# Performance work log

Hardware: AMD Instinct MI355X
Metric: run time of the kernel (lower is better)

Reference implementation:

```python
import jax, jax.numpy as jnp
import numpy as np

EMBED_DIM = 2048
NUM_HEADS = 16
HEAD_DIM = EMBED_DIM // NUM_HEADS  # 128
D_K = 128
SCALE = 1.0 / float(np.sqrt(HEAD_DIM))
LAYER_DEPTH = 6 / 12  # amrpa_layer_idx / n_amrpa_layers
BATCH, SEQ = 2, 2048


def setup_inputs() -> dict:
    key = jax.random.key(0)
    ks = jax.random.split(key, 8)
    return {
        "hidden_states": jax.random.normal(ks[0], (BATCH, SEQ, EMBED_DIM), jnp.float32),
        "c_attn_w": jax.random.normal(ks[1], (EMBED_DIM, 3 * EMBED_DIM), jnp.float32) * 0.02,
        "c_attn_b": jax.random.normal(ks[2], (3 * EMBED_DIM,), jnp.float32) * 0.02,
        "c_proj_w": jax.random.normal(ks[3], (EMBED_DIM, EMBED_DIM), jnp.float32) * 0.02,
        "c_proj_b": jax.random.normal(ks[4], (EMBED_DIM,), jnp.float32) * 0.02,
        "cam_gate": jax.random.normal(ks[5], (D_K,), jnp.float32) * 0.1,
        "cam_w0": jax.random.normal(ks[6], (1,), jnp.float32),
        "cam_w1": jax.random.normal(ks[7], (1,), jnp.float32),
    }


def reference(hidden_states, c_attn_w, c_attn_b, c_proj_w, c_proj_b, cam_gate, cam_w0, cam_w1):
    # GPT2 Conv1D-style fused QKV projection: [B,S,3E]
    qkv = hidden_states @ c_attn_w + c_attn_b
    Q, K, V = jnp.split(qkv, 3, axis=2)  # each [B,S,E]
    # NOTE: faithful to source — attention over the FULL embed dim (no head split),
    # scaled by 1/sqrt(head_dim); causal mask is computed but never applied upstream.
    attn_scores = jnp.einsum('bse,bte->bst', Q, K) * SCALE  # [B,S,S]

    # CAM: sliced low-rank channels
    Q_cam, K_cam, V_cam = Q[:, :, :D_K], K[:, :, :D_K], V[:, :, :D_K]
    # base attention map computed under no_grad in the original
    base_A = jax.lax.stop_gradient(
        jax.nn.softmax(jnp.einsum('bsd,btd->bst', Q_cam, K_cam) * SCALE, axis=-1))
    layer_weight = jax.nn.sigmoid(cam_w0[0] + cam_w1[0] * LAYER_DEPTH)
    cam_ctx = jnp.einsum('bst,btd->bsd', base_A, V_cam)            # [B,S,d_k]
    cam_bias = jnp.einsum('bsd,btd->bst', jnp.tanh(cam_ctx * cam_gate), K_cam)
    cam_bias = cam_bias * (SCALE * layer_weight)                   # cam_mask is all-ones

    final_attn = jax.nn.softmax(attn_scores + cam_bias, axis=-1)
    context = jnp.einsum('bst,bte->bse', final_attn, V)            # [B,S,E]
    output = context @ c_proj_w + c_proj_b                         # resid_dropout is identity (eval)
    return output
```

## Files before the change

kernel.cpp:

```cpp
#include <hip/hip_runtime.h>
#include <hip/hip_bf16.h>

typedef unsigned short u16;
typedef __attribute__((ext_vector_type(8))) __bf16 bf16x8;
typedef __attribute__((ext_vector_type(4))) float f32x4;
typedef __attribute__((ext_vector_type(4))) unsigned short u16x4;

#define SCALE_QK 0.08838834764831845f

__device__ __forceinline__ u16 f2bf(float x) {
  union { float f; unsigned u; } v; v.f = x;
  unsigned r = v.u + 0x7fffu + ((v.u >> 16) & 1u);
  return (u16)(r >> 16);
}

__device__ __forceinline__ void gload_lds16(const u16* g, u16* l) {
  __builtin_amdgcn_global_load_lds(
      (const __attribute__((address_space(1))) unsigned*)g,
      (__attribute__((address_space(3))) unsigned*)l, 16, 0, 0);
}

#define CFENCE() asm volatile("" ::: "memory")
#define WAITV(N) asm volatile("s_waitcnt vmcnt(" #N ")" ::: "memory")

template<bool OUT_BF16, bool HAS_BIAS, bool TWO_SEG>
__global__ __launch_bounds__(512, 2)
void g128q(const u16* __restrict__ A1, int lda1, long sA1,
           const u16* __restrict__ B1, int ldb1, long sB1, int K1,
           const u16* __restrict__ A2, int lda2, long sA2,
           const u16* __restrict__ B2, int ldb2, long sB2, int K2,
           void* __restrict__ Cv, int ldc, long sC,
           float scale, const float* __restrict__ bias, int nbx,
           int mapmode, u16* __restrict__ vTout)
{
  extern __shared__ u16 lds[];
  const int bz = blockIdx.z;
  const int nwg = gridDim.x, orig = blockIdx.x;
  const int q8 = nwg >> 3, r8 = nwg & 7;
  const int xcd = orig & 7, lp = orig >> 3;
  const int wg = (xcd < r8 ? xcd * (q8 + 1) : r8 * (q8 + 1) + (xcd - r8) * q8) + lp;
  int bx, by;
  if (mapmode == 1) {
    const int x = wg / 96, c = wg % 96;
    const int rect = c / 48, i6 = c % 48;
    by = rect * 8 + (i6 & 7);
    bx = x * 6 + (i6 >> 3);
  } else {
    by = wg / nbx; bx = wg % nbx;
  }
  const long m0 = (long)by * 256, n0 = (long)bx * 128;

  const int tid = threadIdx.x, wid = tid >> 6, lane = tid & 63;
  const int wm = wid >> 1, wn = wid & 1;
  const int rl = lane & 15, g = lane >> 4;
  const int xa = rl & 7;
  const int uk0 = ((g ^ xa) << 3);
  const int uk1 = (((4 + g) ^ xa) << 3);

  int aoffb[4], boffb[4];
#pragma unroll
  for (int i = 0; i < 4; ++i) aoffb[i] = (wm * 64 + i * 16 + rl) * 64;
#pragma unroll
  for (int j = 0; j < 4; ++j) boffb[j] = 16384 + (wn * 64 + j * 16 + rl) * 64;

  const int ra = tid >> 3;
  const int xcol = (((tid & 7) ^ ((tid >> 3) & 7)) << 3);

  f32x4 acc[4][4];
#pragma unroll
  for (int i = 0; i < 4; ++i)
#pragma unroll
    for (int j = 0; j < 4; ++j) acc[i][j] = (f32x4){0.f, 0.f, 0.f, 0.f};

  bf16x8 av[2][4], bv[2][2];

#define STG(T_, BO_) { const int k0_ = (T_) << 6;                        \
    gload_lds16(Ab + (long)(ra      ) * lda + k0_ + xcol, lds + (BO_) +         tid * 8); \
    gload_lds16(Ab + (long)(ra +  64) * lda + k0_ + xcol, lds + (BO_) +  4096 + tid * 8); \
    gload_lds16(Ab + (long)(ra + 128) * lda + k0_ + xcol, lds + (BO_) +  8192 + tid * 8); \
    gload_lds16(Ab + (long)(ra + 192) * lda + k0_ + xcol, lds + (BO_) + 12288 + tid * 8); \
    gload_lds16(Bb + (long)(ra      ) * ldb + k0_ + xcol, lds + (BO_) + 16384 + tid * 8); \
    gload_lds16(Bb + (long)(ra +  64) * ldb + k0_ + xcol, lds + (BO_) + 20480 + tid * 8); }
#define RD0(BO_) { const u16* p_ = lds + (BO_);                          \
    _Pragma("unroll") for (int i_ = 0; i_ < 4; ++i_) {                   \
      av[0][i_] = *(const bf16x8*)(p_ + aoffb[i_] + uk0);                \
      av[1][i_] = *(const bf16x8*)(p_ + aoffb[i_] + uk1); }              \
    _Pragma("unroll") for (int j_ = 0; j_ < 2; ++j_) {                   \
      bv[0][j_] = *(const bf16x8*)(p_ + boffb[j_] + uk0);                \
      bv[1][j_] = *(const bf16x8*)(p_ + boffb[j_] + uk1); } }
#define RD1(BO_) { const u16* p_ = lds + (BO_);                          \
    _Pragma("unroll") for (int j_ = 0; j_ < 2; ++j_) {                   \
      bv[0][j_] = *(const bf16x8*)(p_ + boffb[2 + j_] + uk0);            \
      bv[1][j_] = *(const bf16x8*)(p_ + boffb[2 + j_] + uk1); } }
#define MMPH(JB_)                                                        \
    CFENCE(); __builtin_amdgcn_s_barrier();                              \
    asm volatile("s_waitcnt lgkmcnt(0)" ::: "memory");                   \
    __builtin_amdgcn_sched_barrier(0);                                   \
    __builtin_amdgcn_s_setprio(1);                                       \
    _Pragma("unroll") for (int k_ = 0; k_ < 2; ++k_)                     \
      _Pragma("unroll") for (int i_ = 0; i_ < 4; ++i_)                   \
        _Pragma("unroll") for (int j_ = 0; j_ < 2; ++j_)                 \
          acc[i_][(JB_) + j_] = __builtin_amdgcn_mfma_f32_16x16x32_bf16( \
              av[k_][i_], bv[k_][j_], acc[i_][(JB_) + j_], 0, 0, 0);     \
    __builtin_amdgcn_s_setprio(0);                                       \
    CFENCE(); __builtin_amdgcn_s_barrier(); CFENCE();

  const int NSEG = TWO_SEG ? 2 : 1;
#pragma unroll 1
  for (int seg = 0; seg < NSEG; ++seg) {
    const int lda = (seg == 0) ? lda1 : lda2;
    const int ldb = (seg == 0) ? ldb1 : ldb2;
    const int K   = (seg == 0) ? K1 : K2;
    const u16* Ab = ((seg == 0) ? A1 + (long)bz * sA1 : A2 + (long)bz * sA2) + m0 * (long)lda;
    const u16* Bb = ((seg == 0) ? B1 + (long)bz * sB1 : B2 + (long)bz * sB2) + n0 * (long)ldb;
    const int NT = K >> 6;

    STG(0, 0); STG(1, 24576);
    WAITV(6);
    CFENCE(); __builtin_amdgcn_s_barrier(); CFENCE();

    int bo = 0;
#pragma unroll 1
    for (int t = 0; t < NT; ++t) {
      RD0(bo);
      if (t + 2 < NT) {
        int bos = bo - 24576; if (bos < 0) bos = 49152;
        STG(t + 2, bos);
        WAITV(6);
      } else if (t + 1 < NT) {
        WAITV(0);
      }
      MMPH(0)
      RD1(bo);
      MMPH(2)
      bo += 24576; if (bo == 73728) bo = 0;
    }
  }
#undef STG
#undef RD0
#undef RD1
#undef MMPH

  const int r0 = (lane >> 4) << 2;
  const int cL = lane & 15;
#pragma unroll
  for (int i = 0; i < 4; ++i) {
#pragma unroll
    for (int j = 0; j < 4; ++j) {
      const long row = m0 + wm * 64 + i * 16 + r0;
      const long col = n0 + wn * 64 + j * 16 + cL;
      float bvs = 0.f;
      if (HAS_BIAS) bvs = bias[col];
      if (OUT_BF16) {
        u16* Cp = (u16*)Cv + (long)bz * sC;
        if (vTout && col >= 4096) {
          u16x4 tq;
#pragma unroll
          for (int r = 0; r < 4; ++r) tq[r] = f2bf(acc[i][j][r] * scale + bvs);
          *(u16x4*)(vTout + ((long)(row >> 11) * 2048 + (col - 4096)) * 2048 + (row & 2047)) = tq;
        } else {
#pragma unroll
          for (int r = 0; r < 4; ++r)
            Cp[(row + r) * ldc + col] = f2bf(acc[i][j][r] * scale + bvs);
        }
      } else {
        float* Cp = (float*)Cv + (long)bz * sC;
#pragma unroll
        for (int r = 0; r < 4; ++r)
          Cp[(row + r) * ldc + col] = acc[i][j][r] * scale + bvs;
      }
    }
  }
}

__global__ __launch_bounds__(256)
void gemm_bt_splitk(const u16* __restrict__ A, int lda, long sA,
                    const u16* __restrict__ B, int ldb, long sB,
                    float* __restrict__ C, int ldc, long sC,
                    int Kslice, float scale)
{
  __shared__ u16 As[128 * 64];
  __shared__ u16 Bs[128 * 64];
  const int ks = blockIdx.z & 7;
  const int bz = blockIdx.z >> 3;
  const u16* Ap  = A + (long)bz * sA + ks * Kslice;
  const u16* Bp  = B + (long)bz * sB + ks * Kslice;
  const int tid  = threadIdx.x;
  const int wid  = tid >> 6;
  const int lane = tid & 63;
  const long m0  = (long)blockIdx.y * 128;
  const long n0  = (long)blockIdx.x * 128;
  const int lrow = lane >> 3;
  const int lk   = (lane & 7) << 3;
  const int wr   = wid >> 1, wc = wid & 1;

  f32x4 acc[4][4];
#pragma unroll
  for (int i = 0; i < 4; ++i)
#pragma unroll
    for (int j = 0; j < 4; ++j) acc[i][j] = (f32x4){0.f, 0.f, 0.f, 0.f};

  for (int k0 = 0; k0 < Kslice; k0 += 64) {
#pragma unroll
    for (int c4 = 0; c4 < 4; ++c4) {
      const int chunk = (wid << 2) + c4;
      gload_lds16(Ap + (m0 + (chunk << 3) + lrow) * lda + k0 + lk, &As[chunk << 9]);
      gload_lds16(Bp + (n0 + (chunk << 3) + lrow) * ldb + k0 + lk, &Bs[chunk << 9]);
    }
    __syncthreads();
#pragma unroll
    for (int kk = 0; kk < 2; ++kk) {
      bf16x8 af[4], bfr[4];
      const int kof   = (kk << 5) + ((lane >> 4) << 3);
      const int rbase = lane & 15;
#pragma unroll
      for (int i = 0; i < 4; ++i)
        af[i] = *(const bf16x8*)&As[(((wr << 6) + (i << 4) + rbase) << 6) + kof];
#pragma unroll
      for (int j = 0; j < 4; ++j)
        bfr[j] = *(const bf16x8*)&Bs[(((wc << 6) + (j << 4) + rbase) << 6) + kof];
#pragma unroll
      for (int i = 0; i < 4; ++i)
#pragma unroll
        for (int j = 0; j < 4; ++j)
          acc[i][j] = __builtin_amdgcn_mfma_f32_16x16x32_bf16(af[i], bfr[j], acc[i][j], 0, 0, 0);
    }
    __syncthreads();
  }

  const int r0 = (lane >> 4) << 2;
  const int cL = lane & 15;
  float* Cp = C + (long)bz * sC;
#pragma unroll
  for (int i = 0; i < 4; ++i) {
#pragma unroll
    for (int j = 0; j < 4; ++j) {
      const long row = m0 + (wr << 6) + (i << 4) + r0;
      const long col = n0 + (wc << 6) + (j << 4) + cL;
#pragma unroll
      for (int r = 0; r < 4; ++r)
        atomicAdd(&Cp[(row + r) * ldc + col], acc[i][j][r] * scale);
    }
  }
}

__global__ __launch_bounds__(256)
void softmax_rows2048(const float* __restrict__ src, u16* __restrict__ dst) {
  const long row = blockIdx.x;
  const float4* s = (const float4*)(src + row * 2048);
  const int tid = threadIdx.x;
  float4 a = s[tid * 2], b = s[tid * 2 + 1];
  float m = fmaxf(fmaxf(fmaxf(a.x, a.y), fmaxf(a.z, a.w)),
                  fmaxf(fmaxf(b.x, b.y), fmaxf(b.z, b.w)));
#pragma unroll
  for (int o = 32; o > 0; o >>= 1) m = fmaxf(m, __shfl_xor(m, o));
  __shared__ float redm[4];
  __shared__ float reds[4];
  if ((tid & 63) == 0) redm[tid >> 6] = m;
  __syncthreads();
  m = fmaxf(fmaxf(redm[0], redm[1]), fmaxf(redm[2], redm[3]));
  float e[8];
  e[0] = __expf(a.x - m); e[1] = __expf(a.y - m); e[2] = __expf(a.z - m); e[3] = __expf(a.w - m);
  e[4] = __expf(b.x - m); e[5] = __expf(b.y - m); e[6] = __expf(b.z - m); e[7] = __expf(b.w - m);
  float sum = e[0] + e[1] + e[2] + e[3] + e[4] + e[5] + e[6] + e[7];
#pragma unroll
  for (int o = 32; o > 0; o >>= 1) sum += __shfl_xor(sum, o);
  if ((tid & 63) == 0) reds[tid >> 6] = sum;
  __syncthreads();
  sum = reds[0] + reds[1] + reds[2] + reds[3];
  const float inv = 1.f / sum;
  u16x4 o1 = { f2bf(e[0] * inv), f2bf(e[1] * inv), f2bf(e[2] * inv), f2bf(e[3] * inv) };
  u16x4 o2 = { f2bf(e[4] * inv), f2bf(e[5] * inv), f2bf(e[6] * inv), f2bf(e[7] * inv) };
  u16x4* d = (u16x4*)(dst + row * 2048);
  d[tid * 2]     = o1;
  d[tid * 2 + 1] = o2;
}

__global__ void transpose_f32_to_bf16(const float* __restrict__ src, u16* __restrict__ dst,
                                      int R, int C) {
  __shared__ float t[32][33];
  const int c0 = blockIdx.x * 32, r0 = blockIdx.y * 32;
  const int tx = threadIdx.x, ty = threadIdx.y;
#pragma unroll
  for (int i = 0; i < 4; ++i)
    t[ty + i * 8][tx] = src[(long)(r0 + ty + i * 8) * C + c0 + tx];
  __syncthreads();
#pragma unroll
  for (int i = 0; i < 4; ++i)
    dst[(long)(c0 + ty + i * 8) * R + r0 + tx] = f2bf(t[tx][ty + i * 8]);
}

__global__ __launch_bounds__(256)
void convert_f32_to_bf16(const float* __restrict__ src, u16* __restrict__ dst, long n4) {
  long i = (long)blockIdx.x * 256 + threadIdx.x;
  if (i < n4) {
    float4 v = ((const float4*)src)[i];
    *(u16x4*)(dst + i * 4) = (u16x4){ f2bf(v.x), f2bf(v.y), f2bf(v.z), f2bf(v.w) };
  }
}

__global__ __launch_bounds__(256)
void cam_tanh_kernel(const float* __restrict__ ctx, const float* __restrict__ gate,
                     const float* __restrict__ w0, const float* __restrict__ w1,
                     u16* __restrict__ out, int n) {
  int i = blockIdx.x * 256 + threadIdx.x;
  if (i < n) {
    const float lw = 1.f / (1.f + __expf(-(w0[0] + 0.5f * w1[0])));
    int d = i & 127;
    out[i] = f2bf(tanhf(ctx[i] * gate[d]) * lw);
  }
}

__global__ __launch_bounds__(256)
void zero_f32(float* __restrict__ p, int n) {
  int i = blockIdx.x * 256 + threadIdx.x;
  if (i < n) p[i] = 0.f;
}

extern "C" void kernel_launch(void* const* d_in, const int* in_sizes, int n_in,
                              void* d_out, int out_size, void* d_ws, size_t ws_size,
                              hipStream_t stream) {
  const float* hs       = (const float*)d_in[0];
  const float* c_attn_w = (const float*)d_in[1];
  const float* c_attn_b = (const float*)d_in[2];
  const float* c_proj_w = (const float*)d_in[3];
  const float* c_proj_b = (const float*)d_in[4];
  const float* cam_gate = (const float*)d_in[5];
  const float* cam_w0   = (const float*)d_in[6];
  const float* cam_w1   = (const float*)d_in[7];
  float* out = (float*)d_out;

  char* w = (char*)d_ws;
  u16*   hs_b    = (u16*)(w + 256);
  u16*   waT_b   = (u16*)(w + 256 + 16777216UL);
  u16*   wpT_b   = (u16*)(w + 256 + 41943040UL);
  u16*   qkv_b   = (u16*)(w + 256 + 50331648UL);
  u16*   vT_b    = (u16*)(w + 256 + 100663296UL);
  float* scoresF = (float*)(w + 256 + 117440512UL);
  float* camS    = (float*)(w + 256 + 150994944UL);
  float* ctxF    = (float*)(w + 256 + 184549376UL);
  u16*   camT_b  = (u16*)(w + 256 + 186646528UL);
  u16* baseA_b = hs_b;
  u16* P_b     = (u16*)camS;
  u16* ctxE_b  = (u16*)scoresF;

  dim3 b256(256);
  const int LDSB = 147456;

  hipFuncSetAttribute((const void*)g128q<true, true, false>,
                      hipFuncAttributeMaxDynamicSharedMemorySize, LDSB);
  hipFuncSetAttribute((const void*)g128q<false, false, false>,
                      hipFuncAttributeMaxDynamicSharedMemorySize, LDSB);
  hipFuncSetAttribute((const void*)g128q<false, false, true>,
                      hipFuncAttributeMaxDynamicSharedMemorySize, LDSB);
  hipFuncSetAttribute((const void*)g128q<true, false, false>,
                      hipFuncAttributeMaxDynamicSharedMemorySize, LDSB);
  hipFuncSetAttribute((const void*)g128q<false, true, false>,
                      hipFuncAttributeMaxDynamicSharedMemorySize, LDSB);

  convert_f32_to_bf16<<<dim3(8192), b256, 0, stream>>>(hs, hs_b, 2097152L);
  transpose_f32_to_bf16<<<dim3(192, 64), dim3(32, 8), 0, stream>>>(c_attn_w, waT_b, 2048, 6144);
  transpose_f32_to_bf16<<<dim3(64, 64), dim3(32, 8), 0, stream>>>(c_proj_w, wpT_b, 2048, 2048);

  g128q<true, true, false><<<dim3(768, 1, 1), dim3(512), LDSB, stream>>>(
      hs_b, 2048, 0L, waT_b, 2048, 0L, 2048,
      nullptr, 0, 0L, nullptr, 0, 0L, 0,
      qkv_b, 6144, 0L, 1.f, c_attn_b, 48, 1, vT_b);

  g128q<false, false, false><<<dim3(128, 1, 2), dim3(512), LDSB, stream>>>(
      qkv_b, 6144, 2048L * 6144, qkv_b + 2048, 6144, 2048L * 6144, 128,
      nullptr, 0, 0L, nullptr, 0, 0L, 0,
      camS, 2048, 2048L * 2048, SCALE_QK, nullptr, 16, 0, nullptr);

  softmax_rows2048<<<dim3(4096), b256, 0, stream>>>(camS, baseA_b);

  zero_f32<<<dim3(2048), b256, 0, stream>>>(ctxF, 524288);
  gemm_bt_splitk<<<dim3(1, 16, 16), b256, 0, stream>>>(
      baseA_b, 2048, 2048L * 2048, vT_b, 2048, 2048L * 2048,
      ctxF, 128, 2048L * 128, 256, 1.f);

  cam_tanh_kernel<<<dim3(2048), b256, 0, stream>>>(ctxF, cam_gate, cam_w0, cam_w1,
                                                   camT_b, 524288);

  g128q<false, false, true><<<dim3(128, 1, 2), dim3(512), LDSB, stream>>>(
      qkv_b, 6144, 2048L * 6144, qkv_b + 2048, 6144, 2048L * 6144, 2048,
      camT_b, 128, 2048L * 128, qkv_b + 2048, 6144, 2048L * 6144, 128,
      scoresF, 2048, 2048L * 2048, SCALE_QK, nullptr, 16, 0, nullptr);

  softmax_rows2048<<<dim3(4096), b256, 0, stream>>>(scoresF, P_b);

  g128q<true, false, false><<<dim3(128, 1, 2), dim3(512), LDSB, stream>>>(
      P_b, 2048, 2048L * 2048, vT_b, 2048, 2048L * 2048, 2048,
      nullptr, 0, 0L, nullptr, 0, 0L, 0,
      ctxE_b, 2048, 2048L * 2048, 1.f, nullptr, 16, 0, nullptr);

  g128q<false, true, false><<<dim3(256, 1, 1), dim3(512), LDSB, stream>>>(
      ctxE_b, 2048, 0L, wpT_b, 2048, 0L, 2048,
      nullptr, 0, 0L, nullptr, 0, 0L, 0,
      out, 2048, 0L, 1.f, c_proj_b, 16, 0, nullptr);
}
```

Baseline: 332.1 us.

## Add dedicated QKV projection GEMM with 4-stage K=32 LDS pipeline

Adds a specialized single-segment GEMM kernel, used only for the fused QKV projection. It stages 32-wide K slices into a four-deep LDS ring through direct global-to-LDS loads, swapping register fragments between iterations, with 96KB of LDS instead of 144KB. The aim is more overlap of loads with MFMA work on the largest GEMM, plus possibly lower LDS pressure. The other GEMMs keep the existing kernel with its mapping and transpose-output arguments removed. Smaller K steps mean more barriers per unit of work.

```diff
diff --git a/kernel.cpp b/kernel.cpp
--- a/kernel.cpp
+++ b/kernel.cpp
@@ -23,12 +23,10 @@
 #define CFENCE() asm volatile("" ::: "memory")
 #define WAITV(N) asm volatile("s_waitcnt vmcnt(" #N ")" ::: "memory")
 
-template<bool OUT_BF16, bool HAS_BIAS, bool TWO_SEG>
+template<bool OUT_BF16, bool HAS_BIAS>
 __global__ __launch_bounds__(512, 2)
-void g128q(const u16* __restrict__ A1, int lda1, long sA1,
-           const u16* __restrict__ B1, int ldb1, long sB1, int K1,
-           const u16* __restrict__ A2, int lda2, long sA2,
-           const u16* __restrict__ B2, int ldb2, long sB2, int K2,
+void g128p(const u16* __restrict__ A1, int lda, long sA1,
+           const u16* __restrict__ B1, int ldb, long sB1, int K,
            void* __restrict__ Cv, int ldc, long sC,
            float scale, const float* __restrict__ bias, int nbx,
            int mapmode, u16* __restrict__ vTout)
@@ -48,6 +46,133 @@
   } else {
     by = wg / nbx; bx = wg % nbx;
   }
+  const long m0 = (long)by * 256, n0 = (long)bx * 128;
+
+  const int tid = threadIdx.x, wid = tid >> 6, lane = tid & 63;
+  const int wm = wid >> 1, wn = wid & 1;
+  const int rl = lane & 15, g = lane >> 4;
+  const int sw = ((g ^ ((rl >> 1) & 3)) << 3);
+
+  int aoff[4], boff[4];
+#pragma unroll
+  for (int i = 0; i < 4; ++i) aoff[i] = (wm * 64 + i * 16 + rl) * 32 + sw;
+#pragma unroll
+  for (int j = 0; j < 4; ++j) boff[j] = (wn * 64 + j * 16 + rl) * 32 + sw;
+
+  const int srow = tid >> 2;
+  const int scolX = (((tid & 3) ^ ((srow >> 1) & 3)) << 3);
+
+  f32x4 acc[4][4];
+#pragma unroll
+  for (int i = 0; i < 4; ++i)
+#pragma unroll
+    for (int j = 0; j < 4; ++j) acc[i][j] = (f32x4){0.f, 0.f, 0.f, 0.f};
+
+  bf16x8 avA[4], bvA[4], avB[4], bvB[4];
+
+  const u16* Ab = A1 + (long)bz * sA1 + m0 * (long)lda;
+  const u16* Bb = B1 + (long)bz * sB1 + n0 * (long)ldb;
+
+#define STG(H_) {                                                        \
+    const int h_ = (H_);                                                 \
+    const u16* sa_ = Ab + (long)srow * lda + h_ * 32 + scolX;            \
+    u16* da_ = lds + ((h_ & 3) * 8192) + tid * 8;                        \
+    gload_lds16(sa_, da_);                                               \
+    gload_lds16(sa_ + (long)128 * lda, da_ + 4096);                      \
+    gload_lds16(Bb + (long)srow * ldb + h_ * 32 + scolX,                 \
+                lds + 32768 + ((h_ & 3) * 4096) + tid * 8); }
+#define RD(H_, AV, BV) {                                                 \
+    const u16* aS_ = lds + (((H_) & 3) * 8192);                          \
+    const u16* bS_ = lds + 32768 + (((H_) & 3) * 4096);                  \
+    _Pragma("unroll") for (int i_ = 0; i_ < 4; ++i_)                     \
+      AV[i_] = *(const bf16x8*)(aS_ + aoff[i_]);                         \
+    _Pragma("unroll") for (int j_ = 0; j_ < 4; ++j_)                     \
+      BV[j_] = *(const bf16x8*)(bS_ + boff[j_]); }
+#define BODY(K_, CAV, CBV, NAV, NBV, W_STMT, DO_RD, DO_ST)               \
+    W_STMT;                                                              \
+    CFENCE(); __builtin_amdgcn_s_barrier(); CFENCE();                    \
+    asm volatile("s_waitcnt lgkmcnt(0)" ::: "memory");                   \
+    __builtin_amdgcn_sched_barrier(0);                                   \
+    __builtin_amdgcn_s_setprio(1);                                       \
+    _Pragma("unroll") for (int i_ = 0; i_ < 4; ++i_)                     \
+      _Pragma("unroll") for (int j_ = 0; j_ < 4; ++j_)                   \
+        acc[i_][j_] = __builtin_amdgcn_mfma_f32_16x16x32_bf16(           \
+            CAV[i_], CBV[j_], acc[i_][j_], 0, 0, 0);                     \
+    __builtin_amdgcn_s_setprio(0);                                       \
+    if (DO_RD) { RD((K_) + 1, NAV, NBV); }                               \
+    if (DO_ST) { STG((K_) + 4); }                                        \
+    CFENCE();
+
+  const int H = K >> 5;
+
+  STG(0); STG(1); STG(2);
+  WAITV(6);
+  CFENCE(); __builtin_amdgcn_s_barrier(); CFENCE();
+  RD(0, avA, bvA);
+  STG(3);
+  CFENCE();
+
+#pragma unroll 1
+  for (int k = 0; k + 5 < H; k += 2) {
+    BODY(k,     avA, bvA, avB, bvB, WAITV(6), true, true);
+    BODY(k + 1, avB, bvB, avA, bvA, WAITV(6), true, true);
+  }
+  BODY(H - 4, avA, bvA, avB, bvB, WAITV(6), true,  false);
+  BODY(H - 3, avB, bvB, avA, bvA, WAITV(3), true,  false);
+  BODY(H - 2, avA, bvA, avB, bvB, WAITV(0), true,  false);
+  BODY(H - 1, avB, bvB, avA, bvA, (void)0,  false, false);
+#undef STG
+#undef RD
+#undef BODY
+
+  const int r0 = (lane >> 4) << 2;
+  const int cL = lane & 15;
+#pragma unroll
+  for (int i = 0; i < 4; ++i) {
+#pragma unroll
+    for (int j = 0; j < 4; ++j) {
+      const long row = m0 + wm * 64 + i * 16 + r0;
+      const long col = n0 + wn * 64 + j * 16 + cL;
+      float bvs = 0.f;
+      if (HAS_BIAS) bvs = bias[col];
+      if (OUT_BF16) {
+        u16* Cp = (u16*)Cv + (long)bz * sC;
+        if (vTout && col >= 4096) {
+          u16x4 tq;
+#pragma unroll
+          for (int r = 0; r < 4; ++r) tq[r] = f2bf(acc[i][j][r] * scale + bvs);
+          *(u16x4*)(vTout + ((long)(row >> 11) * 2048 + (col - 4096)) * 2048 + (row & 2047)) = tq;
+        } else {
+#pragma unroll
+          for (int r = 0; r < 4; ++r)
+            Cp[(row + r) * ldc + col] = f2bf(acc[i][j][r] * scale + bvs);
+        }
+      } else {
+        float* Cp = (float*)Cv + (long)bz * sC;
+#pragma unroll
+        for (int r = 0; r < 4; ++r)
+          Cp[(row + r) * ldc + col] = acc[i][j][r] * scale + bvs;
+      }
+    }
+  }
+}
+
+template<bool OUT_BF16, bool HAS_BIAS, bool TWO_SEG>
+__global__ __launch_bounds__(512, 2)
+void g128q(const u16* __restrict__ A1, int lda1, long sA1,
+           const u16* __restrict__ B1, int ldb1, long sB1, int K1,
+           const u16* __restrict__ A2, int lda2, long sA2,
+           const u16* __restrict__ B2, int ldb2, long sB2, int K2,
+           void* __restrict__ Cv, int ldc, long sC,
+           float scale, const float* __restrict__ bias, int nbx)
+{
+  extern __shared__ u16 lds[];
+  const int bz = blockIdx.z;
+  const int nwg = gridDim.x, orig = blockIdx.x;
+  const int q8 = nwg >> 3, r8 = nwg & 7;
+  const int xcd = orig & 7, lp = orig >> 3;
+  const int wg = (xcd < r8 ? xcd * (q8 + 1) : r8 * (q8 + 1) + (xcd - r8) * q8) + lp;
+  const int bx = wg % nbx, by = wg / nbx;
   const long m0 = (long)by * 256, n0 = (long)bx * 128;
 
   const int tid = threadIdx.x, wid = tid >> 6, lane = tid & 63;
@@ -153,16 +278,9 @@
       if (HAS_BIAS) bvs = bias[col];
       if (OUT_BF16) {
         u16* Cp = (u16*)Cv + (long)bz * sC;
-        if (vTout && col >= 4096) {
-          u16x4 tq;
-#pragma unroll
-          for (int r = 0; r < 4; ++r) tq[r] = f2bf(acc[i][j][r] * scale + bvs);
-          *(u16x4*)(vTout + ((long)(row >> 11) * 2048 + (col - 4096)) * 2048 + (row & 2047)) = tq;
-        } else {
-#pragma unroll
-          for (int r = 0; r < 4; ++r)
-            Cp[(row + r) * ldc + col] = f2bf(acc[i][j][r] * scale + bvs);
-        }
+#pragma unroll
+        for (int r = 0; r < 4; ++r)
+          Cp[(row + r) * ldc + col] = f2bf(acc[i][j][r] * scale + bvs);
       } else {
         float* Cp = (float*)Cv + (long)bz * sC;
 #pragma unroll
@@ -345,32 +463,32 @@
   u16* ctxE_b  = (u16*)scoresF;
 
   dim3 b256(256);
-  const int LDSB = 147456;
-
-  hipFuncSetAttribute((const void*)g128q<true, true, false>,
-                      hipFuncAttributeMaxDynamicSharedMemorySize, LDSB);
+  const int LDSP = 98304;
+  const int LDSQ = 147456;
+
+  hipFuncSetAttribute((const void*)g128p<true, true>,
+                      hipFuncAttributeMaxDynamicSharedMemorySize, LDSP);
   hipFuncSetAttribute((const void*)g128q<false, false, false>,
-                      hipFuncAttributeMaxDynamicSharedMemorySize, LDSB);
+                      hipFuncAttributeMaxDynamicSharedMemorySize, LDSQ);
   hipFuncSetAttribute((const void*)g128q<false, false, true>,
-                      hipFuncAttributeMaxDynamicSharedMemorySize, LDSB);
+                      hipFuncAttributeMaxDynamicSharedMemorySize, LDSQ);
   hipFuncSetAttribute((const void*)g128q<true, false, false>,
-                      hipFuncAttributeMaxDynamicSharedMemorySize, LDSB);
+                      hipFuncAttributeMaxDynamicSharedMemorySize, LDSQ);
   hipFuncSetAttribute((const void*)g128q<false, true, false>,
-                      hipFuncAttributeMaxDynamicSharedMemorySize, LDSB);
+                      hipFuncAttributeMaxDynamicSharedMemorySize, LDSQ);
 
   convert_f32_to_bf16<<<dim3(8192), b256, 0, stream>>>(hs, hs_b, 2097152L);
   transpose_f32_to_bf16<<<dim3(192, 64), dim3(32, 8), 0, stream>>>(c_attn_w, waT_b, 2048, 6144);
   transpose_f32_to_bf16<<<dim3(64, 64), dim3(32, 8), 0, stream>>>(c_proj_w, wpT_b, 2048, 2048);
 
-  g128q<true, true, false><<<dim3(768, 1, 1), dim3(512), LDSB, stream>>>(
+  g128p<true, true><<<dim3(768, 1, 1), dim3(512), LDSP, stream>>>(
       hs_b, 2048, 0L, waT_b, 2048, 0L, 2048,
-      nullptr, 0, 0L, nullptr, 0, 0L, 0,
       qkv_b, 6144, 0L, 1.f, c_attn_b, 48, 1, vT_b);
 
-  g128q<false, false, false><<<dim3(128, 1, 2), dim3(512), LDSB, stream>>>(
+  g128q<false, false, false><<<dim3(128, 1, 2), dim3(512), LDSQ, stream>>>(
       qkv_b, 6144, 2048L * 6144, qkv_b + 2048, 6144, 2048L * 6144, 128,
       nullptr, 0, 0L, nullptr, 0, 0L, 0,
-      camS, 2048, 2048L * 2048, SCALE_QK, nullptr, 16, 0, nullptr);
+      camS, 2048, 2048L * 2048, SCALE_QK, nullptr, 16);
 
   softmax_rows2048<<<dim3(4096), b256, 0, stream>>>(camS, baseA_b);
 
@@ -382,20 +500,20 @@
   cam_tanh_kernel<<<dim3(2048), b256, 0, stream>>>(ctxF, cam_gate, cam_w0, cam_w1,
                                                    camT_b, 524288);
 
-  g128q<false, false, true><<<dim3(128, 1, 2), dim3(512), LDSB, stream>>>(
+  g128q<false, false, true><<<dim3(128, 1, 2), dim3(512), LDSQ, stream>>>(
       qkv_b, 6144, 2048L * 6144, qkv_b + 2048, 6144, 2048L * 6144, 2048,
       camT_b, 128, 2048L * 128, qkv_b + 2048, 6144, 2048L * 6144, 128,
-      scoresF, 2048, 2048L * 2048, SCALE_QK, nullptr, 16, 0, nullptr);
+      scoresF, 2048, 2048L * 2048, SCALE_QK, nullptr, 16);
 
   softmax_rows2048<<<dim3(4096), b256, 0, stream>>>(scoresF, P_b);
 
-  g128q<true, false, false><<<dim3(128, 1, 2), dim3(512), LDSB, stream>>>(
+  g128q<true, false, false><<<dim3(128, 1, 2), dim3(512), LDSQ, stream>>>(
       P_b, 2048, 2048L * 2048, vT_b, 2048, 2048L * 2048, 2048,
       nullptr, 0, 0L, nullptr, 0, 0L, 0,
-      ctxE_b, 2048, 2048L * 2048, 1.f, nullptr, 16, 0, nullptr);
-
-  g128q<false, true, false><<<dim3(256, 1, 1), dim3(512), LDSB, stream>>>(
+      ctxE_b, 2048, 2048L * 2048, 1.f, nullptr, 16);
+
+  g128q<false, true, false><<<dim3(256, 1, 1), dim3(512), LDSQ, stream>>>(
       ctxE_b, 2048, 0L, wpT_b, 2048, 0L, 2048,
       nullptr, 0, 0L, nullptr, 0, 0L, 0,
-      out, 2048, 0L, 1.f, c_proj_b, 16, 0, nullptr);
-}
+      out, 2048, 0L, 1.f, c_proj_b, 16);
+}
```

Measured after the change: 341.4 us (median of 2 runs). 1.03x slower.
